# Kernel tuning notes

Hardware: AMD Instinct MI355X
Metric: run time of the kernel (lower is better)

Reference implementation:

```python
import jax, jax.numpy as jnp
import numpy as np

K = 9          # kernel_size
PAD = K // 2   # same padding
SIGMA = 1.0
EPS = 1e-5     # BatchNorm eps


def setup_inputs() -> dict:
    key = jax.random.key(0)
    k0, k1, k2 = jax.random.split(key, 3)
    B, Cin, Cout, L = 4, 64, 64, 131072
    x = jax.random.normal(k0, (B, Cin, L), jnp.float32)
    coords = jax.random.uniform(k1, (B, 3, L), jnp.float32)  # 3D point coords in [0,1)
    W = jax.random.normal(k2, (Cout, Cin, K), jnp.float32) * (1.0 / np.sqrt(Cin * K))
    bias = jnp.zeros((Cout,), jnp.float32)
    gamma = jnp.ones((Cout,), jnp.float32)
    beta = jnp.zeros((Cout,), jnp.float32)
    return {"x": x, "coords": coords, "W": W, "bias": bias, "gamma": gamma, "beta": beta}


def reference(x, coords, W, bias, gamma, beta):
    B, Cin, L = x.shape
    # zero-pad sequence dim for 'same' conv
    xpad = jnp.pad(x, ((0, 0), (0, 0), (PAD, PAD)))
    cpad = jnp.pad(coords, ((0, 0), (0, 0), (PAD, PAD)))
    # unfold: neighbor windows of size K (K is a small compile-time constant)
    x_unf = jnp.stack([xpad[:, :, k:k + L] for k in range(K)], axis=2)   # [B,Cin,K,L]
    c_unf = jnp.stack([cpad[:, :, k:k + L] for k in range(K)], axis=2)   # [B,3,K,L]
    # Gaussian spatial weights from coord distances (WeightedConv1D)
    dist2 = jnp.sum((c_unf - coords[:, :, None, :]) ** 2, axis=1)        # [B,K,L]
    w = jnp.exp(-dist2 / (2.0 * SIGMA * SIGMA))                          # [B,K,L]
    # weighted conv: contract over (Cin, K)
    out = jnp.einsum('ock,bckl->bol', W, x_unf * w[:, None, :, :])       # [B,Cout,L]
    out = out + bias[None, :, None]
    # BatchNorm1d (training-mode batch statistics over B and L) + ReLU
    mean = out.mean(axis=(0, 2), keepdims=True)
    var = out.var(axis=(0, 2), keepdims=True)
    out = (out - mean) * jax.lax.rsqrt(var + EPS)
    out = out * gamma[None, :, None] + beta[None, :, None]
    return jax.nn.relu(out)
```

## Files before the change

### kernel.cpp

```cpp
#include <hip/hip_runtime.h>
#include <hip/hip_bf16.h>

#define KK 9
#define PADK 4
#define CIN 64
#define COUT 64
#define LSEQ 131072
#define NB 4
#define TILEL 128
#define XROWS 136
#define XRS 72
#define NTILES 1024
#define NPART 64

typedef __attribute__((ext_vector_type(8))) short v8s;
typedef __attribute__((ext_vector_type(4))) float v4f;

__device__ __forceinline__ unsigned short f2bf(float f) {
  __hip_bfloat16 h = __float2bfloat16(f);
  return *reinterpret_cast<unsigned short*>(&h);
}
__device__ __forceinline__ float bf2f(unsigned short s) {
  return __uint_as_float(((unsigned)s) << 16);
}

__device__ __forceinline__ void store_o(float* p, float v) { *p = v; }
__device__ __forceinline__ void store_o(__hip_bfloat16* p, float v) { *p = __float2bfloat16(v); }

__global__ void wtrans_kernel(const float* __restrict__ W, v8s* __restrict__ Wt) {
  int t = blockIdx.x * 256 + threadIdx.x;
  if (t >= KK * 2 * 4 * 64) return;
  int lane = t & 63;
  int frag = t >> 6;
  int mblk = frag & 3;
  int s    = (frag >> 2) & 1;
  int k    = frag >> 3;
  int m = lane & 15, q = lane >> 4;
  int o = mblk * 16 + m;
  union { v8s v; unsigned short h[8]; } u;
#pragma unroll
  for (int j = 0; j < 8; ++j) {
    int c = 32 * s + q * 8 + j;
    u.h[j] = f2bf(W[(o * CIN + c) * KK + k]);
  }
  Wt[t] = u.v;
}

template <typename OutT>
__global__ __launch_bounds__(256, 4)
void conv_kernel(const float* __restrict__ x, const float* __restrict__ coords,
                 const v8s* __restrict__ Wt, OutT* __restrict__ cv,
                 float* __restrict__ stat_sum, float* __restrict__ stat_sq) {
  __shared__ __align__(16) __hip_bfloat16 xt[XROWS][XRS];
  __shared__ float wt[KK][TILEL];

  const int tid  = threadIdx.x;
  const int wv   = tid >> 6;
  const int wo   = wv & 1;
  const int wl   = wv >> 1;
  const int lane = tid & 63;
  const int gw   = blockIdx.x;
  const int b    = gw >> 10;
  const int tile = gw & (NTILES - 1);
  const int l0   = tile * TILEL;
  const float* xb = x + (b * CIN) * LSEQ;
  const float* cb = coords + (b * 3) * LSEQ;
  const int m = lane & 15;
  const int q = lane >> 4;

  {
    int cg = tid & 7;
    int lc = tid >> 3;
    int c8 = cg * 8;
    float4 f[8];
#pragma unroll
    for (int t = 0; t < 8; ++t)
      f[t] = *(const float4*)(xb + (c8 + t) * LSEQ + l0 + 4 * lc);
    const float* fp = (const float*)&f[0];
#pragma unroll
    for (int j = 0; j < 4; ++j) {
      union { v8s v; unsigned short h[8]; } u;
#pragma unroll
      for (int t = 0; t < 8; ++t) u.h[t] = f2bf(fp[4 * t + j]);
      *(v8s*)&xt[4 + 4 * lc + j][c8] = u.v;
    }
  }
  if (tid < 128) {
    int side = tid >> 6;
    int c = tid & 63;
    if (side == 0) {
      float el[4] = {0.f, 0.f, 0.f, 0.f};
      if (tile != 0) {
#pragma unroll
        for (int j = 0; j < 4; ++j) el[j] = xb[c * LSEQ + l0 - 4 + j];
      }
#pragma unroll
      for (int j = 0; j < 4; ++j) xt[j][c] = __float2bfloat16(el[j]);
    } else {
      float er[4] = {0.f, 0.f, 0.f, 0.f};
      if (tile != NTILES - 1) {
#pragma unroll
        for (int j = 0; j < 4; ++j) er[j] = xb[c * LSEQ + l0 + TILEL + j];
      }
#pragma unroll
      for (int j = 0; j < 4; ++j) xt[128 + 4 + j][c] = __float2bfloat16(er[j]);
    }
  }
  if (tid < TILEL) {
    int n = tid;
    float sx = cb[l0 + n];
    float sy = cb[LSEQ + l0 + n];
    float sz = cb[2 * LSEQ + l0 + n];
    float w9[KK];
#pragma unroll
    for (int k = 0; k < KK; ++k) {
      int l = l0 + n + k - PADK;
      float cx = 0.f, cy = 0.f, cz = 0.f;
      if ((unsigned)l < (unsigned)LSEQ) {
        cx = cb[l]; cy = cb[LSEQ + l]; cz = cb[2 * LSEQ + l];
      }
      float dx = cx - sx, dy = cy - sy, dz = cz - sz;
      w9[k] = __expf(-0.5f * (dx * dx + dy * dy + dz * dz));
    }
#pragma unroll
    for (int k = 0; k < KK; ++k)
      wt[k][n] = w9[k] - ((k < KK - 1) ? w9[k + 1] : 0.f);
  }
  __syncthreads();

  v4f y[2][4], tot[2][4];
#pragma unroll
  for (int i = 0; i < 2; ++i)
#pragma unroll
    for (int j = 0; j < 4; ++j) {
      y[i][j]   = (v4f){0.f, 0.f, 0.f, 0.f};
      tot[i][j] = (v4f){0.f, 0.f, 0.f, 0.f};
    }

  const v8s* wp = Wt + (wo * 2) * 64 + lane;

#pragma unroll 1
  for (int k = 0; k < KK; ++k) {
#pragma unroll
    for (int s = 0; s < 2; ++s) {
      v8s a0 = wp[k * 512 + s * 256];
      v8s a1 = wp[k * 512 + s * 256 + 64];
#pragma unroll
      for (int nbq = 0; nbq < 4; ++nbq) {
        v8s bf = *(const v8s*)&xt[wl * 64 + nbq * 16 + m + k][q * 8 + 32 * s];
        y[0][nbq] = __builtin_amdgcn_mfma_f32_16x16x32_bf16(a0, bf, y[0][nbq], 0, 0, 0);
        y[1][nbq] = __builtin_amdgcn_mfma_f32_16x16x32_bf16(a1, bf, y[1][nbq], 0, 0, 0);
      }
    }
#pragma unroll
    for (int nbq = 0; nbq < 4; ++nbq) {
      float d = wt[k][wl * 64 + nbq * 16 + m];
#pragma unroll
      for (int mb = 0; mb < 2; ++mb)
#pragma unroll
        for (int r = 0; r < 4; ++r)
          tot[mb][nbq][r] = __builtin_fmaf(d, y[mb][nbq][r], tot[mb][nbq][r]);
    }
  }

  const int part = gw & (NPART - 1);
  OutT* outb = cv + (b * COUT) * LSEQ;
#pragma unroll
  for (int mb = 0; mb < 2; ++mb) {
#pragma unroll
    for (int r = 0; r < 4; ++r) {
      int o = wo * 32 + mb * 16 + q * 4 + r;
      float s1 = 0.f, s2 = 0.f;
#pragma unroll
      for (int nbq = 0; nbq < 4; ++nbq) {
        float v = tot[mb][nbq][r];
        s1 += v;
        s2 += v * v;
        store_o(&outb[o * LSEQ + l0 + wl * 64 + nbq * 16 + m], v);
      }
#pragma unroll
      for (int off = 1; off < 16; off <<= 1) {
        s1 += __shfl_xor(s1, off, 64);
        s2 += __shfl_xor(s2, off, 64);
      }
      if (m == 0) {
        atomicAdd(&stat_sum[part * COUT + o], s1);
        atomicAdd(&stat_sq [part * COUT + o], s2);
      }
    }
  }
}

__global__ void finalize_kernel(const float* __restrict__ stat_sum,
                                const float* __restrict__ stat_sq,
                                const float* __restrict__ gamma,
                                const float* __restrict__ beta,
                                float* __restrict__ ss) {
  int o = threadIdx.x;
  float s1 = 0.f, s2 = 0.f;
  for (int p = 0; p < NPART; ++p) {
    s1 += stat_sum[p * COUT + o];
    s2 += stat_sq [p * COUT + o];
  }
  const float invN = 1.0f / (float)(NB * LSEQ);
  float mean = s1 * invN;
  float var  = s2 * invN - mean * mean;
  float sc = gamma[o] * rsqrtf(var + 1e-5f);
  ss[o]        = sc;
  ss[COUT + o] = beta[o] - mean * sc;
}

__global__ __launch_bounds__(256)
void scale_f32_kernel(float* __restrict__ data, const float* __restrict__ ss) {
  const int blk = blockIdx.x;
  const int ch = (blk >> 6) & 63;
  const float sc = ss[ch];
  const float sh = ss[COUT + ch];
  const int base = blk * 2048 + threadIdx.x * 8;
  float4 a = *(float4*)(data + base);
  float4 b = *(float4*)(data + base + 4);
  a.x = fmaxf(fmaf(a.x, sc, sh), 0.f);
  a.y = fmaxf(fmaf(a.y, sc, sh), 0.f);
  a.z = fmaxf(fmaf(a.z, sc, sh), 0.f);
  a.w = fmaxf(fmaf(a.w, sc, sh), 0.f);
  b.x = fmaxf(fmaf(b.x, sc, sh), 0.f);
  b.y = fmaxf(fmaf(b.y, sc, sh), 0.f);
  b.z = fmaxf(fmaf(b.z, sc, sh), 0.f);
  b.w = fmaxf(fmaf(b.w, sc, sh), 0.f);
  *(float4*)(data + base)     = a;
  *(float4*)(data + base + 4) = b;
}

__global__ __launch_bounds__(256)
void scale_bf16_kernel(const __hip_bfloat16* __restrict__ cvin,
                       const float* __restrict__ ss, float* __restrict__ out) {
  const int blk = blockIdx.x;
  const int ch = (blk >> 6) & 63;
  const float sc = ss[ch];
  const float sh = ss[COUT + ch];
  const int base = blk * 2048 + threadIdx.x * 8;
  union { v8s v; unsigned short h[8]; } u;
  u.v = *(const v8s*)(cvin + base);
  float r[8];
#pragma unroll
  for (int i = 0; i < 8; ++i)
    r[i] = fmaxf(fmaf(bf2f(u.h[i]), sc, sh), 0.f);
  *(float4*)(out + base)     = make_float4(r[0], r[1], r[2], r[3]);
  *(float4*)(out + base + 4) = make_float4(r[4], r[5], r[6], r[7]);
}

extern "C" void kernel_launch(void* const* d_in, const int* in_sizes, int n_in,
                              void* d_out, int out_size, void* d_ws, size_t ws_size,
                              hipStream_t stream) {
  const float* x      = (const float*)d_in[0];
  const float* coords = (const float*)d_in[1];
  const float* W      = (const float*)d_in[2];
  const float* gamma  = (const float*)d_in[4];
  const float* beta   = (const float*)d_in[5];
  float* out = (float*)d_out;
  char* ws = (char*)d_ws;

  float* stat_sum = (float*)(ws);
  float* stat_sq  = (float*)(ws + 16384);
  float* ss       = (float*)(ws + 32768);
  v8s*   Wt       = (v8s*)(ws + 40960);
  __hip_bfloat16* scratch = (__hip_bfloat16*)(ws + 131072);

  const size_t need_bf16 = (size_t)131072 + (size_t)NB * COUT * LSEQ * 2;
  const bool bf16_path = ws_size >= need_bf16;

  hipMemsetAsync(ws, 0, 32768, stream);
  wtrans_kernel<<<18, 256, 0, stream>>>(W, Wt);

  if (bf16_path) {
    conv_kernel<__hip_bfloat16><<<NB * NTILES, 256, 0, stream>>>(
        x, coords, Wt, scratch, stat_sum, stat_sq);
    finalize_kernel<<<1, COUT, 0, stream>>>(stat_sum, stat_sq, gamma, beta, ss);
    scale_bf16_kernel<<<(NB * COUT * (LSEQ / 2048)), 256, 0, stream>>>(scratch, ss, out);
  } else {
    conv_kernel<float><<<NB * NTILES, 256, 0, stream>>>(
        x, coords, Wt, out, stat_sum, stat_sq);
    finalize_kernel<<<1, COUT, 0, stream>>>(stat_sum, stat_sq, gamma, beta, ss);
    scale_f32_kernel<<<(NB * COUT * (LSEQ / 2048)), 256, 0, stream>>>(out, ss);
  }
}
```

Before: 322.8 us.

## Make conv blocks persistent over four tiles with double-buffered register prefetch

Each conv block now handles four consecutive sequence tiles instead of one, using double-buffered LDS tiles. The global loads of x, halo and coords for the next tile are issued into registers before the MFMA loop of the current tile, so memory latency overlaps compute. The Gaussian weight work is spread over all 256 threads by giving each thread half of the 9 taps, and the halo loads become float4 loads. The prefetch registers raise register pressure, so launch bounds drop to 3 blocks per SM. The grid shrinks to a quarter of its old size, which could reduce load balance across CUs.

```diff
diff --git a/kernel.cpp b/kernel.cpp
--- a/kernel.cpp
+++ b/kernel.cpp
@@ -12,6 +12,8 @@
 #define XRS 72
 #define NTILES 1024
 #define NPART 64
+#define TPB 4
+#define GRIDC (NB * NTILES / TPB)
 
 typedef __attribute__((ext_vector_type(8))) short v8s;
 typedef __attribute__((ext_vector_type(4))) float v4f;
@@ -47,145 +49,170 @@
 }
 
 template <typename OutT>
-__global__ __launch_bounds__(256, 4)
+__global__ __launch_bounds__(256, 3)
 void conv_kernel(const float* __restrict__ x, const float* __restrict__ coords,
                  const v8s* __restrict__ Wt, OutT* __restrict__ cv,
                  float* __restrict__ stat_sum, float* __restrict__ stat_sq) {
-  __shared__ __align__(16) __hip_bfloat16 xt[XROWS][XRS];
-  __shared__ float wt[KK][TILEL];
+  __shared__ __align__(16) __hip_bfloat16 xt[2][XROWS][XRS];
+  __shared__ float wt[2][KK][TILEL];
 
   const int tid  = threadIdx.x;
   const int wv   = tid >> 6;
   const int wo   = wv & 1;
   const int wl   = wv >> 1;
   const int lane = tid & 63;
-  const int gw   = blockIdx.x;
-  const int b    = gw >> 10;
-  const int tile = gw & (NTILES - 1);
-  const int l0   = tile * TILEL;
+  const int m = lane & 15;
+  const int q = lane >> 4;
+
+  const int bid = blockIdx.x;
+  const int b   = bid >> 8;
+  const int t0  = (bid & 255) * TPB;
   const float* xb = x + (b * CIN) * LSEQ;
   const float* cb = coords + (b * 3) * LSEQ;
-  const int m = lane & 15;
-  const int q = lane >> 4;
-
-  {
-    int cg = tid & 7;
-    int lc = tid >> 3;
-    int c8 = cg * 8;
-    float4 f[8];
+  OutT* outb = cv + (b * COUT) * LSEQ;
+
+  const int cg = tid & 7, lc = tid >> 3, c8 = cg * 8;
+  const int cn = tid >> 1;
+  const int khalf = tid & 1;
+  const int k0 = khalf * 4;
+
+  float4 f[8];
+  float4 hx;
+  float sx, sy, sz;
+  float cxk[5], cyk[5], czk[5];
+
+  auto prefetch = [&](int tile) {
+    const int l0 = tile * TILEL;
 #pragma unroll
     for (int t = 0; t < 8; ++t)
       f[t] = *(const float4*)(xb + (c8 + t) * LSEQ + l0 + 4 * lc);
-    const float* fp = (const float*)&f[0];
-#pragma unroll
-    for (int j = 0; j < 4; ++j) {
-      union { v8s v; unsigned short h[8]; } u;
-#pragma unroll
-      for (int t = 0; t < 8; ++t) u.h[t] = f2bf(fp[4 * t + j]);
-      *(v8s*)&xt[4 + 4 * lc + j][c8] = u.v;
-    }
-  }
-  if (tid < 128) {
-    int side = tid >> 6;
-    int c = tid & 63;
-    if (side == 0) {
-      float el[4] = {0.f, 0.f, 0.f, 0.f};
-      if (tile != 0) {
-#pragma unroll
-        for (int j = 0; j < 4; ++j) el[j] = xb[c * LSEQ + l0 - 4 + j];
-      }
-#pragma unroll
-      for (int j = 0; j < 4; ++j) xt[j][c] = __float2bfloat16(el[j]);
-    } else {
-      float er[4] = {0.f, 0.f, 0.f, 0.f};
-      if (tile != NTILES - 1) {
-#pragma unroll
-        for (int j = 0; j < 4; ++j) er[j] = xb[c * LSEQ + l0 + TILEL + j];
-      }
-#pragma unroll
-      for (int j = 0; j < 4; ++j) xt[128 + 4 + j][c] = __float2bfloat16(er[j]);
-    }
-  }
-  if (tid < TILEL) {
-    int n = tid;
-    float sx = cb[l0 + n];
-    float sy = cb[LSEQ + l0 + n];
-    float sz = cb[2 * LSEQ + l0 + n];
-    float w9[KK];
-#pragma unroll
-    for (int k = 0; k < KK; ++k) {
-      int l = l0 + n + k - PADK;
+    if (tid < 128) {
+      int side = tid >> 6, c = tid & 63;
+      hx = make_float4(0.f, 0.f, 0.f, 0.f);
+      if (side == 0) {
+        if (tile != 0) hx = *(const float4*)(xb + c * LSEQ + l0 - 4);
+      } else {
+        if (tile != NTILES - 1) hx = *(const float4*)(xb + c * LSEQ + l0 + TILEL);
+      }
+    }
+    sx = cb[l0 + cn];
+    sy = cb[LSEQ + l0 + cn];
+    sz = cb[2 * LSEQ + l0 + cn];
+#pragma unroll
+    for (int i = 0; i < 5; ++i) {
+      int l = l0 + cn + (k0 + i) - PADK;
       float cx = 0.f, cy = 0.f, cz = 0.f;
       if ((unsigned)l < (unsigned)LSEQ) {
         cx = cb[l]; cy = cb[LSEQ + l]; cz = cb[2 * LSEQ + l];
       }
-      float dx = cx - sx, dy = cy - sy, dz = cz - sz;
-      w9[k] = __expf(-0.5f * (dx * dx + dy * dy + dz * dz));
-    }
-#pragma unroll
-    for (int k = 0; k < KK; ++k)
-      wt[k][n] = w9[k] - ((k < KK - 1) ? w9[k + 1] : 0.f);
-  }
-  __syncthreads();
-
-  v4f y[2][4], tot[2][4];
-#pragma unroll
-  for (int i = 0; i < 2; ++i)
-#pragma unroll
-    for (int j = 0; j < 4; ++j) {
-      y[i][j]   = (v4f){0.f, 0.f, 0.f, 0.f};
-      tot[i][j] = (v4f){0.f, 0.f, 0.f, 0.f};
-    }
-
-  const v8s* wp = Wt + (wo * 2) * 64 + lane;
+      cxk[i] = cx; cyk[i] = cy; czk[i] = cz;
+    }
+  };
+
+  prefetch(t0);
 
 #pragma unroll 1
-  for (int k = 0; k < KK; ++k) {
-#pragma unroll
-    for (int s = 0; s < 2; ++s) {
-      v8s a0 = wp[k * 512 + s * 256];
-      v8s a1 = wp[k * 512 + s * 256 + 64];
+  for (int ti = 0; ti < TPB; ++ti) {
+    const int tile = t0 + ti;
+    const int l0 = tile * TILEL;
+    const int cur = ti & 1;
+
+    {
+      const float* fp = (const float*)&f[0];
+#pragma unroll
+      for (int j = 0; j < 4; ++j) {
+        union { v8s v; unsigned short h[8]; } u;
+#pragma unroll
+        for (int t = 0; t < 8; ++t) u.h[t] = f2bf(fp[4 * t + j]);
+        *(v8s*)&xt[cur][4 + 4 * lc + j][c8] = u.v;
+      }
+      if (tid < 128) {
+        int side = tid >> 6, c = tid & 63;
+        int rb = side ? (TILEL + PADK) : 0;
+        xt[cur][rb + 0][c] = __float2bfloat16(hx.x);
+        xt[cur][rb + 1][c] = __float2bfloat16(hx.y);
+        xt[cur][rb + 2][c] = __float2bfloat16(hx.z);
+        xt[cur][rb + 3][c] = __float2bfloat16(hx.w);
+      }
+      float w5[5];
+#pragma unroll
+      for (int i = 0; i < 5; ++i) {
+        float dx = cxk[i] - sx, dy = cyk[i] - sy, dz = czk[i] - sz;
+        w5[i] = __expf(-0.5f * (dx * dx + dy * dy + dz * dz));
+      }
+      if (khalf == 0) {
+#pragma unroll
+        for (int i = 0; i < 4; ++i) wt[cur][i][cn] = w5[i] - w5[i + 1];
+      } else {
+#pragma unroll
+        for (int i = 0; i < 4; ++i) wt[cur][4 + i][cn] = w5[i] - w5[i + 1];
+        wt[cur][8][cn] = w5[4];
+      }
+    }
+
+    if (ti + 1 < TPB) prefetch(tile + 1);
+
+    asm volatile("s_waitcnt lgkmcnt(0)" ::: "memory");
+    __builtin_amdgcn_s_barrier();
+
+    v4f y[2][4], tot[2][4];
+#pragma unroll
+    for (int i = 0; i < 2; ++i)
+#pragma unroll
+      for (int j = 0; j < 4; ++j) {
+        y[i][j]   = (v4f){0.f, 0.f, 0.f, 0.f};
+        tot[i][j] = (v4f){0.f, 0.f, 0.f, 0.f};
+      }
+
+    const v8s* wp = Wt + (wo * 2) * 64 + lane;
+
+#pragma unroll 1
+    for (int k = 0; k < KK; ++k) {
+#pragma unroll
+      for (int s = 0; s < 2; ++s) {
+        v8s a0 = wp[k * 512 + s * 256];
+        v8s a1 = wp[k * 512 + s * 256 + 64];
+#pragma unroll
+        for (int nbq = 0; nbq < 4; ++nbq) {
+          v8s bf = *(const v8s*)&xt[cur][wl * 64 + nbq * 16 + m + k][q * 8 + 32 * s];
+          y[0][nbq] = __builtin_amdgcn_mfma_f32_16x16x32_bf16(a0, bf, y[0][nbq], 0, 0, 0);
+          y[1][nbq] = __builtin_amdgcn_mfma_f32_16x16x32_bf16(a1, bf, y[1][nbq], 0, 0, 0);
+        }
+      }
 #pragma unroll
       for (int nbq = 0; nbq < 4; ++nbq) {
-        v8s bf = *(const v8s*)&xt[wl * 64 + nbq * 16 + m + k][q * 8 + 32 * s];
-        y[0][nbq] = __builtin_amdgcn_mfma_f32_16x16x32_bf16(a0, bf, y[0][nbq], 0, 0, 0);
-        y[1][nbq] = __builtin_amdgcn_mfma_f32_16x16x32_bf16(a1, bf, y[1][nbq], 0, 0, 0);
-      }
-    }
-#pragma unroll
-    for (int nbq = 0; nbq < 4; ++nbq) {
-      float d = wt[k][wl * 64 + nbq * 16 + m];
-#pragma unroll
-      for (int mb = 0; mb < 2; ++mb)
-#pragma unroll
-        for (int r = 0; r < 4; ++r)
-          tot[mb][nbq][r] = __builtin_fmaf(d, y[mb][nbq][r], tot[mb][nbq][r]);
-    }
-  }
-
-  const int part = gw & (NPART - 1);
-  OutT* outb = cv + (b * COUT) * LSEQ;
-#pragma unroll
-  for (int mb = 0; mb < 2; ++mb) {
-#pragma unroll
-    for (int r = 0; r < 4; ++r) {
-      int o = wo * 32 + mb * 16 + q * 4 + r;
-      float s1 = 0.f, s2 = 0.f;
-#pragma unroll
-      for (int nbq = 0; nbq < 4; ++nbq) {
-        float v = tot[mb][nbq][r];
-        s1 += v;
-        s2 += v * v;
-        store_o(&outb[o * LSEQ + l0 + wl * 64 + nbq * 16 + m], v);
-      }
-#pragma unroll
-      for (int off = 1; off < 16; off <<= 1) {
-        s1 += __shfl_xor(s1, off, 64);
-        s2 += __shfl_xor(s2, off, 64);
-      }
-      if (m == 0) {
-        atomicAdd(&stat_sum[part * COUT + o], s1);
-        atomicAdd(&stat_sq [part * COUT + o], s2);
+        float d = wt[cur][k][wl * 64 + nbq * 16 + m];
+#pragma unroll
+        for (int mb = 0; mb < 2; ++mb)
+#pragma unroll
+          for (int r = 0; r < 4; ++r)
+            tot[mb][nbq][r] = __builtin_fmaf(d, y[mb][nbq][r], tot[mb][nbq][r]);
+      }
+    }
+
+    const int part = tile & (NPART - 1);
+#pragma unroll
+    for (int mb = 0; mb < 2; ++mb) {
+#pragma unroll
+      for (int r = 0; r < 4; ++r) {
+        int o = wo * 32 + mb * 16 + q * 4 + r;
+        float s1 = 0.f, s2 = 0.f;
+#pragma unroll
+        for (int nbq = 0; nbq < 4; ++nbq) {
+          float v = tot[mb][nbq][r];
+          s1 += v;
+          s2 += v * v;
+          store_o(&outb[o * LSEQ + l0 + wl * 64 + nbq * 16 + m], v);
+        }
+#pragma unroll
+        for (int off = 1; off < 16; off <<= 1) {
+          s1 += __shfl_xor(s1, off, 64);
+          s2 += __shfl_xor(s2, off, 64);
+        }
+        if (m == 0) {
+          atomicAdd(&stat_sum[part * COUT + o], s1);
+          atomicAdd(&stat_sq [part * COUT + o], s2);
+        }
       }
     }
   }
@@ -273,12 +300,12 @@
   wtrans_kernel<<<18, 256, 0, stream>>>(W, Wt);
 
   if (bf16_path) {
-    conv_kernel<__hip_bfloat16><<<NB * NTILES, 256, 0, stream>>>(
+    conv_kernel<__hip_bfloat16><<<GRIDC, 256, 0, stream>>>(
         x, coords, Wt, scratch, stat_sum, stat_sq);
     finalize_kernel<<<1, COUT, 0, stream>>>(stat_sum, stat_sq, gamma, beta, ss);
     scale_bf16_kernel<<<(NB * COUT * (LSEQ / 2048)), 256, 0, stream>>>(scratch, ss, out);
   } else {
-    conv_kernel<float><<<NB * NTILES, 256, 0, stream>>>(
+    conv_kernel<float><<<GRIDC, 256, 0, stream>>>(
         x, coords, Wt, out, stat_sum, stat_sq);
     finalize_kernel<<<1, COUT, 0, stream>>>(stat_sum, stat_sq, gamma, beta, ss);
     scale_f32_kernel<<<(NB * COUT * (LSEQ / 2048)), 256, 0, stream>>>(out, ss);
```

Result: slower. 342.5 us (+6.1%).

## Fuse conv, BN finalize and scale into one persistent cooperative kernel

Applied to the files above, without the earlier changes.

Replaces the conv, finalize and scale launches with a single cooperative kernel of 512 blocks. Each block processes 8 tiles and prefetches the next tile's x and coords into registers while it computes the current one. After a grid-wide sync, every block finalizes the BN statistics itself and normalizes its own slice, which is still L2-warm. It also switches the 16-lane reductions to DPP adds. The costs are lower occupancy (launch bounds 2), a grid barrier, and extra register pressure from the prefetch; if the cooperative launch fails, the code falls back to the old path.

```diff
diff --git a/kernel.cpp b/kernel.cpp
--- a/kernel.cpp
+++ b/kernel.cpp
@@ -1,5 +1,8 @@
 #include <hip/hip_runtime.h>
 #include <hip/hip_bf16.h>
+#include <hip/hip_cooperative_groups.h>
+
+namespace cg = cooperative_groups;
 
 #define KK 9
 #define PADK 4
@@ -12,6 +15,8 @@
 #define XRS 72
 #define NTILES 1024
 #define NPART 64
+#define TPB 8
+#define GRIDC (NB * NTILES / TPB)
 
 typedef __attribute__((ext_vector_type(8))) short v8s;
 typedef __attribute__((ext_vector_type(4))) float v4f;
@@ -26,6 +31,19 @@
 
 __device__ __forceinline__ void store_o(float* p, float v) { *p = v; }
 __device__ __forceinline__ void store_o(__hip_bfloat16* p, float v) { *p = __float2bfloat16(v); }
+
+template <int CTRL>
+__device__ __forceinline__ float dppadd(float v) {
+  int s = __builtin_amdgcn_update_dpp(0, __float_as_int(v), CTRL, 0xF, 0xF, true);
+  return v + __int_as_float(s);
+}
+__device__ __forceinline__ float red16(float v) {
+  v = dppadd<0xB1>(v);
+  v = dppadd<0x4E>(v);
+  v = dppadd<0x141>(v);
+  v = dppadd<0x140>(v);
+  return v;
+}
 
 __global__ void wtrans_kernel(const float* __restrict__ W, v8s* __restrict__ Wt) {
   int t = blockIdx.x * 256 + threadIdx.x;
@@ -47,10 +65,235 @@
 }
 
 template <typename OutT>
+__global__ __launch_bounds__(256, 2)
+void fused_kernel(const float* __restrict__ x, const float* __restrict__ coords,
+                  const v8s* __restrict__ Wt, OutT* __restrict__ cv,
+                  float* __restrict__ out,
+                  float* __restrict__ stat_sum, float* __restrict__ stat_sq,
+                  const float* __restrict__ gamma, const float* __restrict__ beta) {
+  __shared__ __align__(16) __hip_bfloat16 xt[XROWS][XRS];
+  __shared__ float wt[KK][TILEL];
+
+  const int tid  = threadIdx.x;
+  const int wv   = tid >> 6;
+  const int wo   = wv & 1;
+  const int wl   = wv >> 1;
+  const int lane = tid & 63;
+  const int m = lane & 15;
+  const int q = lane >> 4;
+
+  const int bid = blockIdx.x;
+  const int b   = bid >> 7;
+  const int t0  = (bid & 127) * TPB;
+  const float* xb = x + (b * CIN) * LSEQ;
+  const float* cb = coords + (b * 3) * LSEQ;
+  OutT*  cvb  = cv  + (size_t)(b * COUT) * LSEQ;
+  float* outb = out + (size_t)(b * COUT) * LSEQ;
+
+  const int cg8 = tid & 7, lc = tid >> 3, c8 = cg8 * 8;
+  const int cn = tid & 127, kh = tid >> 7, k0 = kh * 4;
+
+  float4 f[8];
+  float4 hx;
+  float sx, sy, sz;
+  float nx[5], ny[5], nz[5];
+
+  auto prefetch = [&](int tile) {
+    const int l0 = tile * TILEL;
+#pragma unroll
+    for (int t = 0; t < 8; ++t)
+      f[t] = *(const float4*)(xb + (c8 + t) * LSEQ + l0 + 4 * lc);
+    if (tid < 128) {
+      int side = tid >> 6, c = tid & 63;
+      hx = make_float4(0.f, 0.f, 0.f, 0.f);
+      if (side == 0) {
+        if (tile != 0) hx = *(const float4*)(xb + c * LSEQ + l0 - 4);
+      } else {
+        if (tile != NTILES - 1) hx = *(const float4*)(xb + c * LSEQ + l0 + TILEL);
+      }
+    }
+    sx = cb[l0 + cn];
+    sy = cb[LSEQ + l0 + cn];
+    sz = cb[2 * LSEQ + l0 + cn];
+#pragma unroll
+    for (int i = 0; i < 5; ++i) {
+      int l = l0 + cn + (k0 + i) - PADK;
+      float cx = 0.f, cy = 0.f, cz = 0.f;
+      if ((unsigned)l < (unsigned)LSEQ) {
+        cx = cb[l]; cy = cb[LSEQ + l]; cz = cb[2 * LSEQ + l];
+      }
+      nx[i] = cx; ny[i] = cy; nz[i] = cz;
+    }
+  };
+
+  prefetch(t0);
+
+#pragma unroll 1
+  for (int ti = 0; ti < TPB; ++ti) {
+    const int tile = t0 + ti;
+    const int l0 = tile * TILEL;
+
+    {
+      const float* fp = (const float*)&f[0];
+#pragma unroll
+      for (int j = 0; j < 4; ++j) {
+        union { v8s v; unsigned short h[8]; } u;
+#pragma unroll
+        for (int t = 0; t < 8; ++t) u.h[t] = f2bf(fp[4 * t + j]);
+        *(v8s*)&xt[4 + 4 * lc + j][c8] = u.v;
+      }
+      if (tid < 128) {
+        int side = tid >> 6, c = tid & 63;
+        int rb = side ? (TILEL + PADK) : 0;
+        xt[rb + 0][c] = __float2bfloat16(hx.x);
+        xt[rb + 1][c] = __float2bfloat16(hx.y);
+        xt[rb + 2][c] = __float2bfloat16(hx.z);
+        xt[rb + 3][c] = __float2bfloat16(hx.w);
+      }
+      float w5[5];
+#pragma unroll
+      for (int i = 0; i < 5; ++i) {
+        float dx = nx[i] - sx, dy = ny[i] - sy, dz = nz[i] - sz;
+        w5[i] = __expf(-0.5f * (dx * dx + dy * dy + dz * dz));
+      }
+      if (kh == 0) {
+#pragma unroll
+        for (int i = 0; i < 4; ++i) wt[i][cn] = w5[i] - w5[i + 1];
+      } else {
+#pragma unroll
+        for (int i = 0; i < 4; ++i) wt[4 + i][cn] = w5[i] - w5[i + 1];
+        wt[8][cn] = w5[4];
+      }
+    }
+
+    if (ti + 1 < TPB) prefetch(tile + 1);
+
+    asm volatile("s_waitcnt lgkmcnt(0)" ::: "memory");
+    __builtin_amdgcn_s_barrier();
+
+    v4f y[2][4], tot[2][4];
+#pragma unroll
+    for (int i = 0; i < 2; ++i)
+#pragma unroll
+      for (int j = 0; j < 4; ++j) {
+        y[i][j]   = (v4f){0.f, 0.f, 0.f, 0.f};
+        tot[i][j] = (v4f){0.f, 0.f, 0.f, 0.f};
+      }
+
+    const v8s* wp = Wt + (wo * 2) * 64 + lane;
+
+#pragma unroll 1
+    for (int k = 0; k < KK; ++k) {
+#pragma unroll
+      for (int s = 0; s < 2; ++s) {
+        v8s a0 = wp[k * 512 + s * 256];
+        v8s a1 = wp[k * 512 + s * 256 + 64];
+#pragma unroll
+        for (int nbq = 0; nbq < 4; ++nbq) {
+          v8s bf = *(const v8s*)&xt[wl * 64 + nbq * 16 + m + k][q * 8 + 32 * s];
+          y[0][nbq] = __builtin_amdgcn_mfma_f32_16x16x32_bf16(a0, bf, y[0][nbq], 0, 0, 0);
+          y[1][nbq] = __builtin_amdgcn_mfma_f32_16x16x32_bf16(a1, bf, y[1][nbq], 0, 0, 0);
+        }
+      }
+#pragma unroll
+      for (int nbq = 0; nbq < 4; ++nbq) {
+        float d = wt[k][wl * 64 + nbq * 16 + m];
+#pragma unroll
+        for (int mb = 0; mb < 2; ++mb)
+#pragma unroll
+          for (int r = 0; r < 4; ++r)
+            tot[mb][nbq][r] = __builtin_fmaf(d, y[mb][nbq][r], tot[mb][nbq][r]);
+      }
+    }
+
+    const int part = tile & (NPART - 1);
+#pragma unroll
+    for (int mb = 0; mb < 2; ++mb) {
+#pragma unroll
+      for (int r = 0; r < 4; ++r) {
+        int o = wo * 32 + mb * 16 + q * 4 + r;
+        float s1 = 0.f, s2 = 0.f;
+#pragma unroll
+        for (int nbq = 0; nbq < 4; ++nbq) {
+          float v = tot[mb][nbq][r];
+          s1 += v;
+          s2 += v * v;
+          store_o(&cvb[o * LSEQ + l0 + wl * 64 + nbq * 16 + m], v);
+        }
+        s1 = red16(s1);
+        s2 = red16(s2);
+        if (m == 0) {
+          atomicAdd(&stat_sum[part * COUT + o], s1);
+          atomicAdd(&stat_sq [part * COUT + o], s2);
+        }
+      }
+    }
+
+    __builtin_amdgcn_s_barrier();
+  }
+
+  __threadfence();
+  cg::this_grid().sync();
+
+  {
+    float* wtf = &wt[0][0];
+    const int o = tid & 63, pq = tid >> 6;
+    float s1 = 0.f, s2 = 0.f;
+#pragma unroll 4
+    for (int p = pq * 16; p < pq * 16 + 16; ++p) {
+      s1 += stat_sum[p * COUT + o];
+      s2 += stat_sq [p * COUT + o];
+    }
+    wtf[128 + pq * 64 + o] = s1;
+    wtf[384 + pq * 64 + o] = s2;
+    __syncthreads();
+    if (tid < 64) {
+      float t1 = wtf[128 + tid] + wtf[192 + tid] + wtf[256 + tid] + wtf[320 + tid];
+      float t2 = wtf[384 + tid] + wtf[448 + tid] + wtf[512 + tid] + wtf[576 + tid];
+      const float invN = 1.0f / (float)(NB * LSEQ);
+      float mean = t1 * invN;
+      float var  = t2 * invN - mean * mean;
+      float sc = gamma[tid] * rsqrtf(var + 1e-5f);
+      wtf[tid]      = sc;
+      wtf[64 + tid] = beta[tid] - mean * sc;
+    }
+    __syncthreads();
+
+    const int oo = tid >> 2, sg = tid & 3;
+    const float sc = wtf[oo], sh = wtf[64 + oo];
+    const size_t base = (size_t)oo * LSEQ + t0 * TILEL + sg * 256;
+    if constexpr (sizeof(OutT) == 2) {
+      const __hip_bfloat16* src = (const __hip_bfloat16*)cvb;
+#pragma unroll 4
+      for (int j = 0; j < 32; ++j) {
+        union { v8s v; unsigned short h[8]; } u;
+        u.v = *(const v8s*)(src + base + j * 8);
+        float r[8];
+#pragma unroll
+        for (int i = 0; i < 8; ++i)
+          r[i] = fmaxf(fmaf(bf2f(u.h[i]), sc, sh), 0.f);
+        *(float4*)(outb + base + j * 8)     = make_float4(r[0], r[1], r[2], r[3]);
+        *(float4*)(outb + base + j * 8 + 4) = make_float4(r[4], r[5], r[6], r[7]);
+      }
+    } else {
+#pragma unroll 4
+      for (int j = 0; j < 64; ++j) {
+        float4 a = *(float4*)(outb + base + j * 4);
+        a.x = fmaxf(fmaf(a.x, sc, sh), 0.f);
+        a.y = fmaxf(fmaf(a.y, sc, sh), 0.f);
+        a.z = fmaxf(fmaf(a.z, sc, sh), 0.f);
+        a.w = fmaxf(fmaf(a.w, sc, sh), 0.f);
+        *(float4*)(outb + base + j * 4) = a;
+      }
+    }
+  }
+}
+
+template <typename OutT>
 __global__ __launch_bounds__(256, 4)
-void conv_kernel(const float* __restrict__ x, const float* __restrict__ coords,
-                 const v8s* __restrict__ Wt, OutT* __restrict__ cv,
-                 float* __restrict__ stat_sum, float* __restrict__ stat_sq) {
+void conv_fallback(const float* __restrict__ x, const float* __restrict__ coords,
+                   const v8s* __restrict__ Wt, OutT* __restrict__ cv,
+                   float* __restrict__ stat_sum, float* __restrict__ stat_sq) {
   __shared__ __align__(16) __hip_bfloat16 xt[XROWS][XRS];
   __shared__ float wt[KK][TILEL];
 
@@ -164,7 +407,7 @@
   }
 
   const int part = gw & (NPART - 1);
-  OutT* outb = cv + (b * COUT) * LSEQ;
+  OutT* outb = cv + (size_t)(b * COUT) * LSEQ;
 #pragma unroll
   for (int mb = 0; mb < 2; ++mb) {
 #pragma unroll
@@ -178,11 +421,8 @@
         s2 += v * v;
         store_o(&outb[o * LSEQ + l0 + wl * 64 + nbq * 16 + m], v);
       }
-#pragma unroll
-      for (int off = 1; off < 16; off <<= 1) {
-        s1 += __shfl_xor(s1, off, 64);
-        s2 += __shfl_xor(s2, off, 64);
-      }
+      s1 = red16(s1);
+      s2 = red16(s2);
       if (m == 0) {
         atomicAdd(&stat_sum[part * COUT + o], s1);
         atomicAdd(&stat_sq [part * COUT + o], s2);
@@ -272,15 +512,31 @@
   hipMemsetAsync(ws, 0, 32768, stream);
   wtrans_kernel<<<18, 256, 0, stream>>>(W, Wt);
 
+  hipError_t cerr;
   if (bf16_path) {
-    conv_kernel<__hip_bfloat16><<<NB * NTILES, 256, 0, stream>>>(
-        x, coords, Wt, scratch, stat_sum, stat_sq);
-    finalize_kernel<<<1, COUT, 0, stream>>>(stat_sum, stat_sq, gamma, beta, ss);
-    scale_bf16_kernel<<<(NB * COUT * (LSEQ / 2048)), 256, 0, stream>>>(scratch, ss, out);
+    void* args[9] = {(void*)&x, (void*)&coords, (void*)&Wt, (void*)&scratch,
+                     (void*)&out, (void*)&stat_sum, (void*)&stat_sq,
+                     (void*)&gamma, (void*)&beta};
+    cerr = hipLaunchCooperativeKernel((void*)fused_kernel<__hip_bfloat16>,
+                                      dim3(GRIDC), dim3(256), args, 0, stream);
+    if (cerr != hipSuccess) {
+      conv_fallback<__hip_bfloat16><<<NB * NTILES, 256, 0, stream>>>(
+          x, coords, Wt, scratch, stat_sum, stat_sq);
+      finalize_kernel<<<1, COUT, 0, stream>>>(stat_sum, stat_sq, gamma, beta, ss);
+      scale_bf16_kernel<<<(NB * COUT * (LSEQ / 2048)), 256, 0, stream>>>(scratch, ss, out);
+    }
   } else {
-    conv_kernel<float><<<NB * NTILES, 256, 0, stream>>>(
-        x, coords, Wt, out, stat_sum, stat_sq);
-    finalize_kernel<<<1, COUT, 0, stream>>>(stat_sum, stat_sq, gamma, beta, ss);
-    scale_f32_kernel<<<(NB * COUT * (LSEQ / 2048)), 256, 0, stream>>>(out, ss);
-  }
-}
+    float* cvf = out;
+    void* args[9] = {(void*)&x, (void*)&coords, (void*)&Wt, (void*)&cvf,
+                     (void*)&out, (void*)&stat_sum, (void*)&stat_sq,
+                     (void*)&gamma, (void*)&beta};
+    cerr = hipLaunchCooperativeKernel((void*)fused_kernel<float>,
+                                      dim3(GRIDC), dim3(256), args, 0, stream);
+    if (cerr != hipSuccess) {
+      conv_fallback<float><<<NB * NTILES, 256, 0, stream>>>(
+          x, coords, Wt, out, stat_sum, stat_sq);
+      finalize_kernel<<<1, COUT, 0, stream>>>(stat_sum, stat_sq, gamma, beta, ss);
+      scale_f32_kernel<<<(NB * COUT * (LSEQ / 2048)), 256, 0, stream>>>(out, ss);
+    }
+  }
+}
```

Result: slower. 520.1 us (+61.1%).

## Restructure weighted conv MFMA loop to per-tap products instead of prefix-sum differencing

Applied to the files above, without the earlier changes.

Replaces the running-prefix accumulation scheme, which kept y accumulators across taps and applied differenced weights, with per-tap fresh MFMA products scaled directly by the Gaussian weight. This frees the persistent y registers so occupancy is raised to 5 waves per EU. It also swaps the shuffle-based 16-lane reductions for DPP adds and parallelises the finalize kernel across 256 threads. The cost is extra zero-initialised MFMA chains and possible register pressure or spills under the tighter launch bound.

```diff
diff --git a/kernel.cpp b/kernel.cpp
--- a/kernel.cpp
+++ b/kernel.cpp
@@ -27,6 +27,19 @@
 __device__ __forceinline__ void store_o(float* p, float v) { *p = v; }
 __device__ __forceinline__ void store_o(__hip_bfloat16* p, float v) { *p = __float2bfloat16(v); }
 
+template <int CTRL>
+__device__ __forceinline__ float dppadd(float v) {
+  int s = __builtin_amdgcn_update_dpp(0, __float_as_int(v), CTRL, 0xF, 0xF, true);
+  return v + __int_as_float(s);
+}
+__device__ __forceinline__ float red16(float v) {
+  v = dppadd<0xB1>(v);
+  v = dppadd<0x4E>(v);
+  v = dppadd<0x141>(v);
+  v = dppadd<0x140>(v);
+  return v;
+}
+
 __global__ void wtrans_kernel(const float* __restrict__ W, v8s* __restrict__ Wt) {
   int t = blockIdx.x * 256 + threadIdx.x;
   if (t >= KK * 2 * 4 * 64) return;
@@ -47,7 +60,7 @@
 }
 
 template <typename OutT>
-__global__ __launch_bounds__(256, 4)
+__global__ __launch_bounds__(256, 5)
 void conv_kernel(const float* __restrict__ x, const float* __restrict__ coords,
                  const v8s* __restrict__ Wt, OutT* __restrict__ cv,
                  float* __restrict__ stat_sum, float* __restrict__ stat_sq) {
@@ -111,7 +124,6 @@
     float sx = cb[l0 + n];
     float sy = cb[LSEQ + l0 + n];
     float sz = cb[2 * LSEQ + l0 + n];
-    float w9[KK];
 #pragma unroll
     for (int k = 0; k < KK; ++k) {
       int l = l0 + n + k - PADK;
@@ -120,51 +132,47 @@
         cx = cb[l]; cy = cb[LSEQ + l]; cz = cb[2 * LSEQ + l];
       }
       float dx = cx - sx, dy = cy - sy, dz = cz - sz;
-      w9[k] = __expf(-0.5f * (dx * dx + dy * dy + dz * dz));
-    }
-#pragma unroll
-    for (int k = 0; k < KK; ++k)
-      wt[k][n] = w9[k] - ((k < KK - 1) ? w9[k + 1] : 0.f);
+      wt[k][n] = __expf(-0.5f * (dx * dx + dy * dy + dz * dz));
+    }
   }
   __syncthreads();
 
-  v4f y[2][4], tot[2][4];
+  v4f tot[2][4];
 #pragma unroll
   for (int i = 0; i < 2; ++i)
 #pragma unroll
-    for (int j = 0; j < 4; ++j) {
-      y[i][j]   = (v4f){0.f, 0.f, 0.f, 0.f};
+    for (int j = 0; j < 4; ++j)
       tot[i][j] = (v4f){0.f, 0.f, 0.f, 0.f};
-    }
-
+
+  const v4f z4 = (v4f){0.f, 0.f, 0.f, 0.f};
   const v8s* wp = Wt + (wo * 2) * 64 + lane;
 
 #pragma unroll 1
   for (int k = 0; k < KK; ++k) {
-#pragma unroll
-    for (int s = 0; s < 2; ++s) {
-      v8s a0 = wp[k * 512 + s * 256];
-      v8s a1 = wp[k * 512 + s * 256 + 64];
-#pragma unroll
-      for (int nbq = 0; nbq < 4; ++nbq) {
-        v8s bf = *(const v8s*)&xt[wl * 64 + nbq * 16 + m + k][q * 8 + 32 * s];
-        y[0][nbq] = __builtin_amdgcn_mfma_f32_16x16x32_bf16(a0, bf, y[0][nbq], 0, 0, 0);
-        y[1][nbq] = __builtin_amdgcn_mfma_f32_16x16x32_bf16(a1, bf, y[1][nbq], 0, 0, 0);
-      }
-    }
+    v8s a00 = wp[k * 512];
+    v8s a10 = wp[k * 512 + 64];
+    v8s a01 = wp[k * 512 + 256];
+    v8s a11 = wp[k * 512 + 256 + 64];
 #pragma unroll
     for (int nbq = 0; nbq < 4; ++nbq) {
-      float d = wt[k][wl * 64 + nbq * 16 + m];
-#pragma unroll
-      for (int mb = 0; mb < 2; ++mb)
-#pragma unroll
-        for (int r = 0; r < 4; ++r)
-          tot[mb][nbq][r] = __builtin_fmaf(d, y[mb][nbq][r], tot[mb][nbq][r]);
+      const __hip_bfloat16* xr = &xt[wl * 64 + nbq * 16 + m + k][0];
+      v8s bf0 = *(const v8s*)(xr + q * 8);
+      v8s bf1 = *(const v8s*)(xr + q * 8 + 32);
+      float wk = wt[k][wl * 64 + nbq * 16 + m];
+      v4f y0 = __builtin_amdgcn_mfma_f32_16x16x32_bf16(a00, bf0, z4, 0, 0, 0);
+      y0     = __builtin_amdgcn_mfma_f32_16x16x32_bf16(a01, bf1, y0, 0, 0, 0);
+      v4f y1 = __builtin_amdgcn_mfma_f32_16x16x32_bf16(a10, bf0, z4, 0, 0, 0);
+      y1     = __builtin_amdgcn_mfma_f32_16x16x32_bf16(a11, bf1, y1, 0, 0, 0);
+#pragma unroll
+      for (int r = 0; r < 4; ++r) {
+        tot[0][nbq][r] = __builtin_fmaf(wk, y0[r], tot[0][nbq][r]);
+        tot[1][nbq][r] = __builtin_fmaf(wk, y1[r], tot[1][nbq][r]);
+      }
     }
   }
 
   const int part = gw & (NPART - 1);
-  OutT* outb = cv + (b * COUT) * LSEQ;
+  OutT* outb = cv + (size_t)(b * COUT) * LSEQ;
 #pragma unroll
   for (int mb = 0; mb < 2; ++mb) {
 #pragma unroll
@@ -178,11 +186,8 @@
         s2 += v * v;
         store_o(&outb[o * LSEQ + l0 + wl * 64 + nbq * 16 + m], v);
       }
-#pragma unroll
-      for (int off = 1; off < 16; off <<= 1) {
-        s1 += __shfl_xor(s1, off, 64);
-        s2 += __shfl_xor(s2, off, 64);
-      }
+      s1 = red16(s1);
+      s2 = red16(s2);
       if (m == 0) {
         atomicAdd(&stat_sum[part * COUT + o], s1);
         atomicAdd(&stat_sq [part * COUT + o], s2);
@@ -191,23 +196,33 @@
   }
 }
 
-__global__ void finalize_kernel(const float* __restrict__ stat_sum,
-                                const float* __restrict__ stat_sq,
-                                const float* __restrict__ gamma,
-                                const float* __restrict__ beta,
-                                float* __restrict__ ss) {
-  int o = threadIdx.x;
+__global__ __launch_bounds__(256)
+void finalize_kernel(const float* __restrict__ stat_sum,
+                     const float* __restrict__ stat_sq,
+                     const float* __restrict__ gamma,
+                     const float* __restrict__ beta,
+                     float* __restrict__ ss) {
+  __shared__ float red[2][4][COUT];
+  const int o = threadIdx.x & 63, pq = threadIdx.x >> 6;
   float s1 = 0.f, s2 = 0.f;
-  for (int p = 0; p < NPART; ++p) {
+#pragma unroll 4
+  for (int p = pq * 16; p < pq * 16 + 16; ++p) {
     s1 += stat_sum[p * COUT + o];
     s2 += stat_sq [p * COUT + o];
   }
-  const float invN = 1.0f / (float)(NB * LSEQ);
-  float mean = s1 * invN;
-  float var  = s2 * invN - mean * mean;
-  float sc = gamma[o] * rsqrtf(var + 1e-5f);
-  ss[o]        = sc;
-  ss[COUT + o] = beta[o] - mean * sc;
+  red[0][pq][o] = s1;
+  red[1][pq][o] = s2;
+  __syncthreads();
+  if (threadIdx.x < 64) {
+    float t1 = red[0][0][o] + red[0][1][o] + red[0][2][o] + red[0][3][o];
+    float t2 = red[1][0][o] + red[1][1][o] + red[1][2][o] + red[1][3][o];
+    const float invN = 1.0f / (float)(NB * LSEQ);
+    float mean = t1 * invN;
+    float var  = t2 * invN - mean * mean;
+    float sc = gamma[o] * rsqrtf(var + 1e-5f);
+    ss[o]        = sc;
+    ss[COUT + o] = beta[o] - mean * sc;
+  }
 }
 
 __global__ __launch_bounds__(256)
@@ -275,12 +290,12 @@
   if (bf16_path) {
     conv_kernel<__hip_bfloat16><<<NB * NTILES, 256, 0, stream>>>(
         x, coords, Wt, scratch, stat_sum, stat_sq);
-    finalize_kernel<<<1, COUT, 0, stream>>>(stat_sum, stat_sq, gamma, beta, ss);
+    finalize_kernel<<<1, 256, 0, stream>>>(stat_sum, stat_sq, gamma, beta, ss);
     scale_bf16_kernel<<<(NB * COUT * (LSEQ / 2048)), 256, 0, stream>>>(scratch, ss, out);
   } else {
     conv_kernel<float><<<NB * NTILES, 256, 0, stream>>>(
         x, coords, Wt, out, stat_sum, stat_sq);
-    finalize_kernel<<<1, COUT, 0, stream>>>(stat_sum, stat_sq, gamma, beta, ss);
+    finalize_kernel<<<1, 256, 0, stream>>>(stat_sum, stat_sq, gamma, beta, ss);
     scale_f32_kernel<<<(NB * COUT * (LSEQ / 2048)), 256, 0, stream>>>(out, ss);
   }
 }
```

After: 320.5 us. About the same (-0.7%).
